# Optimization experiments

Hardware: AMD Instinct MI355X
Metric: run time of the kernel (lower is better)

## Reference

```python
import jax, jax.numpy as jnp
import numpy as np

B, L, D = 8, 4096, 256
G, K = 64, 8          # n_groups, group_size
N = G * K             # 512 slots
H = 8                 # attention heads
EPS = 1e-5

def _ln(x, g, b):
    m = jnp.mean(x, axis=-1, keepdims=True)
    v = jnp.var(x, axis=-1, keepdims=True)
    return (x - m) * jax.lax.rsqrt(v + EPS) * g + b

def _gelu(x):
    return jax.nn.gelu(x, approximate=False)  # torch nn.GELU default = exact erf

def setup_inputs() -> dict:
    key = jax.random.key(0)
    ks = jax.random.split(key, 24)
    s = 0.02
    d = {
        'X': jax.random.normal(ks[0], (B, L, D), jnp.float32),
        'S': jax.random.normal(ks[1], (B, N, D), jnp.float32),
        'Wg':  jax.random.normal(ks[2], (D, G)) * s,
        'Wk':  jax.random.normal(ks[3], (D, K)) * s,
        'Wm1': jax.random.normal(ks[4], (D, 2*D)) * s, 'bm1': jnp.zeros((2*D,)),
        'Wm2': jax.random.normal(ks[5], (2*D, D)) * s, 'bm2': jnp.zeros((D,)),
        'Wgt1': jax.random.normal(ks[6], (D, D)) * s, 'bgt1': jnp.zeros((D,)),
        'Wgt2': jax.random.normal(ks[7], (D, 1)) * s, 'bgt2': jnp.zeros((1,)),
        'Wqkv': jax.random.normal(ks[8], (D, 3*D)) * s, 'bqkv': jnp.zeros((3*D,)),
        'Wo':  jax.random.normal(ks[9], (D, D)) * s, 'bo': jnp.zeros((D,)),
        'aln_g': jnp.ones((D,)), 'aln_b': jnp.zeros((D,)),
        'Wu1': jax.random.normal(ks[10], (2*D, 2*D)) * s, 'bu1': jnp.zeros((2*D,)),
        'Wu2': jax.random.normal(ks[11], (2*D, D)) * s, 'bu2': jnp.zeros((D,)),
        'ln_g': jnp.ones((D,)), 'ln_b': jnp.zeros((D,)),
    }
    return d

def reference(X, S, Wg, Wk, Wm1, bm1, Wm2, bm2, Wgt1, bgt1, Wgt2, bgt2,
              Wqkv, bqkv, Wo, bo, aln_g, aln_b, Wu1, bu1, Wu2, bu2, ln_g, ln_b):
    # --- hierarchical routing (eval path: argmax one-hot) ---
    msg = _gelu(X @ Wm1 + bm1) @ Wm2 + bm2                 # (B,L,D)
    gate = jax.nn.sigmoid(_gelu(X @ Wgt1 + bgt1) @ Wgt2 + bgt2)  # (B,L,1)
    gm = msg * gate
    gidx = jnp.argmax(X @ Wg, axis=-1)                     # (B,L)
    kidx = jnp.argmax(X @ Wk, axis=-1)                     # (B,L)
    idx = gidx * K + kidx                                  # flat slot id in [0,N)
    full = jax.nn.one_hot(idx, N, dtype=X.dtype)           # (B,L,N)
    incoming = jnp.einsum('bln,bld->bnd', full, gm)        # (B,N,D)
    # --- slot self-attention ---
    qkv = S @ Wqkv + bqkv
    q, k, v = jnp.split(qkv, 3, axis=-1)
    dh = D // H
    q = q.reshape(B, N, H, dh); k = k.reshape(B, N, H, dh); v = v.reshape(B, N, H, dh)
    scores = jnp.einsum('bqhd,bkhd->bhqk', q, k) / jnp.sqrt(jnp.asarray(dh, X.dtype))
    attn = jax.nn.softmax(scores, axis=-1)
    o = jnp.einsum('bhqk,bkhd->bqhd', attn, v).reshape(B, N, D) @ Wo + bo
    S1 = _ln(S + o, aln_g, aln_b)
    # --- update ---
    cat = jnp.concatenate([S1, incoming], axis=-1)         # (B,N,2D)
    S2 = S1 + _gelu(cat @ Wu1 + bu1) @ Wu2 + bu2
    return _ln(S2, ln_g, ln_b)
```

## Files before the change

kernel.cpp:

```cpp
#include <hip/hip_runtime.h>

typedef __bf16 bf16_t;
typedef __bf16 bf16x8 __attribute__((ext_vector_type(8)));
typedef __bf16 bf16x4v __attribute__((ext_vector_type(4)));
typedef __bf16 bf16x2v __attribute__((ext_vector_type(2)));
typedef float f32x4 __attribute__((ext_vector_type(4)));
typedef unsigned long long u64;

#define LN_EPS 1e-5f

__device__ __forceinline__ float erf_fast(float a) {
  const float t = fabsf(a);
  const float s = a * a;
  float r;
  if (t > 0.921875f) {
    float u;
    r = fmaf(-1.72853470e-5f, t, 3.83197126e-4f);
    u = fmaf(-3.88396438e-3f, t, 2.42546219e-2f);
    r = fmaf(r, s, u);
    r = fmaf(r, t, 1.06777877e-1f);
    r = fmaf(r, t, -6.37245935e-1f);
    r = fmaf(r, t, -1.28717512e-1f);
    r = fmaf(r, t, t);
    r = 1.0f - __expf(-r);
    r = copysignf(r, a);
  } else {
    r = -5.96761703e-4f;
    r = fmaf(r, s, 4.99119423e-3f);
    r = fmaf(r, s, -2.67681349e-2f);
    r = fmaf(r, s, 1.12819925e-1f);
    r = fmaf(r, s, -3.76125336e-1f);
    r = fmaf(r, s, 1.28379166e-1f);
    r = fmaf(r, a, a);
  }
  return r;
}

__device__ __forceinline__ float gelu_f(float x) {
  const float h = 0.5f * x;
  return fmaf(h, erf_fast(x * 0.70710678118654752f), h);
}

__device__ __forceinline__ void async16(const bf16_t* g, bf16_t* l) {
  __builtin_amdgcn_global_load_lds(
      (const __attribute__((address_space(1))) void*)g,
      (__attribute__((address_space(3))) void*)l, 16, 0, 0);
}

__global__ __launch_bounds__(256)
void prep_kernel(const float* __restrict__ X, const float* __restrict__ S,
                 const float* __restrict__ Wg, const float* __restrict__ Wk,
                 const float* __restrict__ Wm1, const float* __restrict__ Wgt1,
                 const float* __restrict__ Wm2, const float* __restrict__ Wqkv,
                 const float* __restrict__ Wo, const float* __restrict__ Wu1,
                 const float* __restrict__ Wu2,
                 bf16_t* __restrict__ Xb, bf16_t* __restrict__ Sb,
                 bf16_t* __restrict__ W1t, bf16_t* __restrict__ W2t,
                 bf16_t* __restrict__ Wqkvt, bf16_t* __restrict__ Wot,
                 bf16_t* __restrict__ Wu1t, bf16_t* __restrict__ Wu2t,
                 float4* __restrict__ zbase)
{
  const int bid = blockIdx.x;
  const int t = threadIdx.x;
  if (bid < 2048) {
    const int base = bid * 1024 + t;
#pragma unroll
    for (int j = 0; j < 4; ++j) {
      const int i = base + j * 256;
      const float4 v = ((const float4*)X)[i];
      bf16x4v o; o[0]=(bf16_t)v.x; o[1]=(bf16_t)v.y; o[2]=(bf16_t)v.z; o[3]=(bf16_t)v.w;
      ((bf16x4v*)Xb)[i] = o;
    }
  } else if (bid < 2304) {
    const int base = (bid - 2048) * 1024 + t;
#pragma unroll
    for (int j = 0; j < 4; ++j) {
      const int i = base + j * 256;
      const float4 v = ((const float4*)S)[i];
      bf16x4v o; o[0]=(bf16_t)v.x; o[1]=(bf16_t)v.y; o[2]=(bf16_t)v.z; o[3]=(bf16_t)v.w;
      ((bf16x4v*)Sb)[i] = o;
    }
  } else if (bid < 3200) {
    const int n = bid - 2304;
    const int k = t;
    float v;
    if (n < 512)      v = Wm1[k * 512 + n];
    else if (n < 768) v = Wgt1[k * 256 + (n - 512)];
    else if (n < 832) v = Wg[k * 64 + (n - 768)];
    else if (n < 840) v = Wk[k * 8 + (n - 832)];
    else              v = 0.f;
    W1t[n * 256 + k] = (bf16_t)v;
  } else if (bid < 3456) {
    const int n = bid - 3200;
    for (int k = t; k < 512; k += 256) W2t[n * 512 + k] = (bf16_t)Wm2[k * 256 + n];
  } else if (bid < 4224) {
    const int n = bid - 3456;
    Wqkvt[n * 256 + t] = (bf16_t)Wqkv[t * 768 + n];
  } else if (bid < 4480) {
    const int n = bid - 4224;
    Wot[n * 256 + t] = (bf16_t)Wo[t * 256 + n];
  } else if (bid < 4992) {
    const int n = bid - 4480;
    for (int k = t; k < 512; k += 256) Wu1t[n * 512 + k] = (bf16_t)Wu1[k * 512 + n];
  } else if (bid < 5248) {
    const int n = bid - 4992;
    for (int k = t; k < 512; k += 256) Wu2t[n * 512 + k] = (bf16_t)Wu2[k * 256 + n];
  } else {
    const int base = (bid - 5248) * 1024 + t;
#pragma unroll
    for (int j = 0; j < 4; ++j)
      zbase[base + j * 256] = make_float4(0.f, 0.f, 0.f, 0.f);
  }
}

__global__ __launch_bounds__(256, 2)
void g1qkv_kernel(const bf16_t* __restrict__ A,
                  const bf16_t* __restrict__ Bt,
                  const float* __restrict__ bias, const float* __restrict__ bias2,
                  bf16_t* __restrict__ h1,
                  const float* __restrict__ wgt2, float* __restrict__ gatelin,
                  u64* __restrict__ bitmap,
                  const bf16_t* __restrict__ Sb, const bf16_t* __restrict__ Wqkvt,
                  const float* __restrict__ bqkv, bf16_t* __restrict__ qkvb,
                  bf16_t* __restrict__ Vt)
{
  const int bid = blockIdx.x;
  const int t = threadIdx.x;
  const int w = t >> 6;
  const int lane = t & 63;
  const int wr = w >> 1, wc = w & 1;
  const int quad = lane >> 4, l15 = lane & 15;

  __shared__ bf16_t lA[128 * 32];
  __shared__ bf16_t lB[128 * 32];
  __shared__ float sWg[256];
  __shared__ int sKi[128];

  if (bid >= 1792) {
    const int id = bid - 1792;
    const int m0 = (id & 63) * 64;
    const int n0 = (id >> 6) * 128;

    f32x4 acc[2][4];
#pragma unroll
    for (int mt = 0; mt < 2; ++mt)
#pragma unroll
      for (int nt = 0; nt < 4; ++nt)
        acc[mt][nt] = (f32x4){0.f, 0.f, 0.f, 0.f};

    for (int k0 = 0; k0 < 256; k0 += 32) {
      async16(Sb + (size_t)(m0 + (t >> 2)) * 256 + k0 + (t & 3) * 8,
              lA + (size_t)(t & 192) * 8);
#pragma unroll
      for (int i = 0; i < 2; ++i) {
        const int c = i * 256 + t;
        async16(Wqkvt + (size_t)(n0 + (c >> 2)) * 256 + k0 + (c & 3) * 8,
                lB + (size_t)(i * 256 + (t & 192)) * 8);
      }
      __syncthreads();
      bf16x8 af[2], bfr[4];
      const int ko = quad * 8;
#pragma unroll
      for (int mt = 0; mt < 2; ++mt)
        af[mt] = *(const bf16x8*)&lA[(wr * 32 + mt * 16 + l15) * 32 + ko];
#pragma unroll
      for (int nt = 0; nt < 4; ++nt)
        bfr[nt] = *(const bf16x8*)&lB[(wc * 64 + nt * 16 + l15) * 32 + ko];
#pragma unroll
      for (int mt = 0; mt < 2; ++mt)
#pragma unroll
        for (int nt = 0; nt < 4; ++nt)
          acc[mt][nt] = __builtin_amdgcn_mfma_f32_16x16x32_bf16(bfr[nt], af[mt], acc[mt][nt], 0, 0, 0);
      __syncthreads();
    }

    if (n0 < 512) {
#pragma unroll
      for (int mt = 0; mt < 2; ++mt) {
        const int row = m0 + wr * 32 + mt * 16 + l15;
#pragma unroll
        for (int nt = 0; nt < 4; ++nt) {
          const int colb = n0 + wc * 64 + nt * 16 + quad * 4;
          const float4 bb = *(const float4*)&bqkv[colb];
          bf16x4v o; o[0]=(bf16_t)(acc[mt][nt][0]+bb.x); o[1]=(bf16_t)(acc[mt][nt][1]+bb.y);
          o[2]=(bf16_t)(acc[mt][nt][2]+bb.z); o[3]=(bf16_t)(acc[mt][nt][3]+bb.w);
          *(bf16x4v*)&qkvb[(size_t)row * 768 + colb] = o;
        }
      }
    } else {
#pragma unroll
      for (int mt = 0; mt < 2; ++mt) {
        const int row = m0 + wr * 32 + mt * 16 + l15;
        const int b = row >> 9, key = row & 511;
#pragma unroll
        for (int nt = 0; nt < 4; ++nt) {
          const int colb = n0 + wc * 64 + nt * 16 + quad * 4;
          const int c = colb - 512;
          const int h2 = c >> 5, dh = c & 31;
          const float4 bb = *(const float4*)&bqkv[colb];
          bf16_t* vb = Vt + ((size_t)(b * 8 + h2) * 32 + dh) * 512 + key;
          vb[0]   = (bf16_t)(acc[mt][nt][0] + bb.x);
          vb[512] = (bf16_t)(acc[mt][nt][1] + bb.y);
          vb[1024]= (bf16_t)(acc[mt][nt][2] + bb.z);
          vb[1536]= (bf16_t)(acc[mt][nt][3] + bb.w);
        }
      }
    }
    return;
  }

  const int m0 = (bid & 255) * 128;
  const int by = bid >> 8;
  const int n0 = by * 128;

  if (by >= 4 && by < 6) sWg[t] = wgt2[t];

  f32x4 acc[4][4];
#pragma unroll
  for (int mt = 0; mt < 4; ++mt)
#pragma unroll
    for (int nt = 0; nt < 4; ++nt)
      acc[mt][nt] = (f32x4){0.f, 0.f, 0.f, 0.f};

  const int srow = t >> 2;
  const int schunk = ((t & 3) ^ (srow & 3)) * 8;
  const int ko = ((quad ^ (l15 & 3)) << 3);

  for (int k0 = 0; k0 < 256; k0 += 32) {
#pragma unroll
    for (int i = 0; i < 2; ++i) {
      const int row = i * 64 + srow;
      async16(A + (size_t)(m0 + row) * 256 + k0 + schunk,
              lA + (size_t)(i * 256 + (t & 192)) * 8);
      async16(Bt + (size_t)(n0 + row) * 256 + k0 + schunk,
              lB + (size_t)(i * 256 + (t & 192)) * 8);
    }
    __syncthreads();
    bf16x8 af[4], bfr[4];
#pragma unroll
    for (int mt = 0; mt < 4; ++mt)
      af[mt] = *(const bf16x8*)&lA[(wr * 64 + mt * 16 + l15) * 32 + ko];
#pragma unroll
    for (int nt = 0; nt < 4; ++nt)
      bfr[nt] = *(const bf16x8*)&lB[(wc * 64 + nt * 16 + l15) * 32 + ko];
#pragma unroll
    for (int mt = 0; mt < 4; ++mt)
#pragma unroll
      for (int nt = 0; nt < 4; ++nt)
        acc[mt][nt] = __builtin_amdgcn_mfma_f32_16x16x32_bf16(bfr[nt], af[mt], acc[mt][nt], 0, 0, 0);
    __syncthreads();
  }

  if (by < 4) {
#pragma unroll
    for (int mt = 0; mt < 4; ++mt) {
      const int row = m0 + wr * 64 + mt * 16 + l15;
#pragma unroll
      for (int nt = 0; nt < 4; ++nt) {
        const int colb = n0 + wc * 64 + nt * 16 + quad * 4;
        const float4 bb = *(const float4*)&bias[colb];
        bf16x4v o;
        o[0] = (bf16_t)gelu_f(acc[mt][nt][0] + bb.x);
        o[1] = (bf16_t)gelu_f(acc[mt][nt][1] + bb.y);
        o[2] = (bf16_t)gelu_f(acc[mt][nt][2] + bb.z);
        o[3] = (bf16_t)gelu_f(acc[mt][nt][3] + bb.w);
        *(bf16x4v*)&h1[(size_t)row * 512 + colb] = o;
      }
    }
  } else if (by < 6) {
#pragma unroll
    for (int mt = 0; mt < 4; ++mt) {
      const int row = m0 + wr * 64 + mt * 16 + l15;
      float part = 0.f;
#pragma unroll
      for (int nt = 0; nt < 4; ++nt) {
        const int colb = n0 + wc * 64 + nt * 16 + quad * 4;
        const int c = colb - 512;
        const float4 bb = *(const float4*)&bias2[c];
        part = fmaf(gelu_f(acc[mt][nt][0] + bb.x), sWg[c + 0], part);
        part = fmaf(gelu_f(acc[mt][nt][1] + bb.y), sWg[c + 1], part);
        part = fmaf(gelu_f(acc[mt][nt][2] + bb.z), sWg[c + 2], part);
        part = fmaf(gelu_f(acc[mt][nt][3] + bb.w), sWg[c + 3], part);
      }
      part += __shfl_xor(part, 16, 64);
      part += __shfl_xor(part, 32, 64);
      if (lane < 16) atomicAdd(&gatelin[row], part);
    }
  } else {
    int bi[4];
#pragma unroll
    for (int mt = 0; mt < 4; ++mt) {
      if (wc == 0) {
        float mv = -1e30f; int mi = 0;
#pragma unroll
        for (int nt = 0; nt < 4; ++nt)
#pragma unroll
          for (int j = 0; j < 4; ++j) {
            const int gc = nt * 16 + quad * 4 + j;
            const float v = acc[mt][nt][j];
            if (v > mv || (v == mv && gc < mi)) { mv = v; mi = gc; }
          }
#pragma unroll
        for (int off = 16; off <= 32; off <<= 1) {
          const float ov = __shfl_xor(mv, off, 64);
          const int oi = __shfl_xor(mi, off, 64);
          if (ov > mv || (ov == mv && oi < mi)) { mv = ov; mi = oi; }
        }
        bi[mt] = mi;
      } else {
        float mv = -1e30f; int mi = 0;
        if (quad < 2) {
#pragma unroll
          for (int j = 0; j < 4; ++j) {
            const int kc = quad * 4 + j;
            const float v = acc[mt][0][j];
            if (v > mv || (v == mv && kc < mi)) { mv = v; mi = kc; }
          }
        }
#pragma unroll
        for (int off = 16; off <= 32; off <<= 1) {
          const float ov = __shfl_xor(mv, off, 64);
          const int oi = __shfl_xor(mi, off, 64);
          if (ov > mv || (ov == mv && oi < mi)) { mv = ov; mi = oi; }
        }
        if (lane < 16) sKi[wr * 64 + mt * 16 + l15] = mi;
      }
    }
    __syncthreads();
    if (wc == 0 && lane < 16) {
#pragma unroll
      for (int mt = 0; mt < 4; ++mt) {
        const int rl = wr * 64 + mt * 16 + l15;
        const int row = m0 + rl;
        const int idx = bi[mt] * 8 + sKi[rl];
        const int b = row >> 12, tok = row & 4095;
        atomicOr(&bitmap[(size_t)(b * 512 + idx) * 64 + (tok >> 6)],
                 1ull << (tok & 63));
      }
    }
  }
}

__global__ __launch_bounds__(256)
void gather_kernel(const bf16_t* __restrict__ h1, const float* __restrict__ gatelin,
                   const float* __restrict__ bgt2, const u64* __restrict__ bitmap,
                   bf16_t* __restrict__ H, float* __restrict__ sumg)
{
  const int bs = blockIdx.x;
  const int b = bs >> 9;
  const int t = threadIdx.x;
  const int w = t >> 6, lane = t & 63;
  __shared__ u64 sw[64];
  __shared__ float pa[4][512];
  __shared__ float psg[4];
  if (t < 64) sw[t] = bitmap[(size_t)bs * 64 + t];
  __syncthreads();
  const float bg = bgt2[0];

  float a[8];
#pragma unroll
  for (int j = 0; j < 8; ++j) a[j] = 0.f;
  float sg = 0.f;

  int wd = w * 16;
  const int wend = wd + 16;
  u64 word = sw[wd];
  auto pop = [&]() -> int {
    while (word == 0) {
      if (++wd >= wend) return -1;
      word = sw[wd];
    }
    const int bit = __builtin_ctzll(word);
    word &= word - 1;
    return (b << 12) + (wd << 6) + bit;
  };

  int l0 = pop();
  float gl0 = 0.f;
  bf16x8 hv0 = {};
  if (l0 >= 0) {
    gl0 = gatelin[l0];
    hv0 = *(const bf16x8*)&h1[(size_t)l0 * 512 + lane * 8];
  }
  while (l0 >= 0) {
    const int l1 = pop();
    float gl1 = 0.f;
    bf16x8 hv1 = {};
    if (l1 >= 0) {
      gl1 = gatelin[l1];
      hv1 = *(const bf16x8*)&h1[(size_t)l1 * 512 + lane * 8];
    }
    const float g = 1.0f / (1.0f + __expf(-(gl0 + bg)));
#pragma unroll
    for (int j = 0; j < 8; ++j) a[j] = fmaf(g, (float)hv0[j], a[j]);
    sg += g;
    l0 = l1; gl0 = gl1; hv0 = hv1;
  }

#pragma unroll
  for (int j = 0; j < 8; ++j) pa[w][lane * 8 + j] = a[j];
  if (lane == 0) psg[w] = sg;
  __syncthreads();

  const int c = t * 2;
  const float r0 = pa[0][c] + pa[1][c] + pa[2][c] + pa[3][c];
  const float r1 = pa[0][c + 1] + pa[1][c + 1] + pa[2][c + 1] + pa[3][c + 1];
  bf16x2v o; o[0] = (bf16_t)r0; o[1] = (bf16_t)r1;
  *(bf16x2v*)&H[(size_t)bs * 512 + c] = o;
  if (t == 0) sumg[bs] = psg[0] + psg[1] + psg[2] + psg[3];
}

__global__ __launch_bounds__(256)
void g2attn_kernel(const bf16_t* __restrict__ qkv, const bf16_t* __restrict__ Vt,
                   bf16_t* __restrict__ obuf,
                   const bf16_t* __restrict__ H, const bf16_t* __restrict__ W2t,
                   const float* __restrict__ bm2, const float* __restrict__ sumg,
                   float* __restrict__ incom)
{
  const int bid = blockIdx.x;
  const int t = threadIdx.x;
  const int w = t >> 6, lane = t & 63;
  const int quad = lane >> 4, l15 = lane & 15;

  __shared__ bf16_t sP[32 * 520];
  __shared__ float sL[32];

  if (bid < 128) {
    const int wr = w >> 1, wc = w & 1;
    const int m0 = (bid & 63) * 64;
    const int n0 = (bid >> 6) * 128;
    bf16_t* lA = sP;
    bf16_t* lB = sP + 64 * 32;

    f32x4 acc[2][4];
#pragma unroll
    for (int mt = 0; mt < 2; ++mt)
#pragma unroll
      for (int nt = 0; nt < 4; ++nt)
        acc[mt][nt] = (f32x4){0.f, 0.f, 0.f, 0.f};

    for (int k0 = 0; k0 < 512; k0 += 32) {
      async16(H + (size_t)(m0 + (t >> 2)) * 512 + k0 + (t & 3) * 8,
              lA + (size_t)(t & 192) * 8);
#pragma unroll
      for (int i = 0; i < 2; ++i) {
        const int c = i * 256 + t;
        async16(W2t + (size_t)(n0 + (c >> 2)) * 512 + k0 + (c & 3) * 8,
                lB + (size_t)(i * 256 + (t & 192)) * 8);
      }
      __syncthreads();
      bf16x8 af[2], bfr[4];
      const int ko = quad * 8;
#pragma unroll
      for (int mt = 0; mt < 2; ++mt)
        af[mt] = *(const bf16x8*)&lA[(wr * 32 + mt * 16 + l15) * 32 + ko];
#pragma unroll
      for (int nt = 0; nt < 4; ++nt)
        bfr[nt] = *(const bf16x8*)&lB[(wc * 64 + nt * 16 + l15) * 32 + ko];
#pragma unroll
      for (int mt = 0; mt < 2; ++mt)
#pragma unroll
        for (int nt = 0; nt < 4; ++nt)
          acc[mt][nt] = __builtin_amdgcn_mfma_f32_16x16x32_bf16(bfr[nt], af[mt], acc[mt][nt], 0, 0, 0);
      __syncthreads();
    }

#pragma unroll
    for (int mt = 0; mt < 2; ++mt) {
      const int row = m0 + wr * 32 + mt * 16 + l15;
      const float gt = sumg[row];
#pragma unroll
      for (int nt = 0; nt < 4; ++nt) {
        const int colb = n0 + wc * 64 + nt * 16 + quad * 4;
        const float4 bb = *(const float4*)&bm2[colb];
        *(float4*)&incom[(size_t)row * 256 + colb] =
            make_float4(fmaf(gt, bb.x, acc[mt][nt][0]), fmaf(gt, bb.y, acc[mt][nt][1]),
                        fmaf(gt, bb.z, acc[mt][nt][2]), fmaf(gt, bb.w, acc[mt][nt][3]));
      }
    }
    return;
  }

  const int abid = bid - 128;
  const int qc = abid & 15;
  const int h = (abid >> 4) & 7;
  const int b = abid >> 7;

  bf16x8 qf[2];
#pragma unroll
  for (int mt = 0; mt < 2; ++mt) {
    const int row = b * 512 + qc * 32 + mt * 16 + l15;
    qf[mt] = *(const bf16x8*)&qkv[(size_t)row * 768 + h * 32 + quad * 8];
  }
  const float scale = 0.17677669529663687f;
  for (int kt = w; kt < 32; kt += 4) {
    const int key = b * 512 + kt * 16 + l15;
    const bf16x8 kf = *(const bf16x8*)&qkv[(size_t)key * 768 + 256 + h * 32 + quad * 8];
#pragma unroll
    for (int mt = 0; mt < 2; ++mt) {
      f32x4 c = (f32x4){0.f, 0.f, 0.f, 0.f};
      c = __builtin_amdgcn_mfma_f32_16x16x32_bf16(qf[mt], kf, c, 0, 0, 0);
#pragma unroll
      for (int r = 0; r < 4; ++r)
        sP[(mt * 16 + quad * 4 + r) * 520 + kt * 16 + l15] = (bf16_t)(c[r] * scale);
    }
  }
  __syncthreads();

#pragma unroll
  for (int ri = 0; ri < 8; ++ri) {
    const int row = w * 8 + ri;
    const bf16x8 sv = *(const bf16x8*)&sP[row * 520 + lane * 8];
    float sval[8];
    float mx = -1e30f;
#pragma unroll
    for (int j = 0; j < 8; ++j) { sval[j] = (float)sv[j]; mx = fmaxf(mx, sval[j]); }
#pragma unroll
    for (int off = 32; off; off >>= 1) mx = fmaxf(mx, __shfl_xor(mx, off, 64));
    float sum = 0.f;
    bf16x8 pv;
#pragma unroll
    for (int j = 0; j < 8; ++j) { const float e = __expf(sval[j] - mx); sum += e; pv[j] = (bf16_t)e; }
#pragma unroll
    for (int off = 32; off; off >>= 1) sum += __shfl_xor(sum, off, 64);
    *(bf16x8*)&sP[row * 520 + lane * 8] = pv;
    if (lane == 0) sL[row] = sum;
  }
  __syncthreads();

  const int wq = w >> 1, wd = w & 1;
  const bf16_t* vbase = Vt + ((size_t)(b * 8 + h) * 32 + wd * 16 + l15) * 512;
  const bf16_t* pbase = &sP[(wq * 16 + l15) * 520];
  f32x4 oacc = (f32x4){0.f, 0.f, 0.f, 0.f};
#pragma unroll
  for (int kt = 0; kt < 16; ++kt) {
    const bf16x8 af = *(const bf16x8*)&pbase[kt * 32 + quad * 8];
    const bf16x8 vf = *(const bf16x8*)&vbase[kt * 32 + quad * 8];
    oacc = __builtin_amdgcn_mfma_f32_16x16x32_bf16(vf, af, oacc, 0, 0, 0);
  }
  const int rowq = wq * 16 + l15;
  const float inv = 1.0f / sL[rowq];
  bf16x4v o;
#pragma unroll
  for (int r = 0; r < 4; ++r) o[r] = (bf16_t)(oacc[r] * inv);
  *(bf16x4v*)&obuf[(size_t)(b * 512 + qc * 32 + rowq) * 256 + h * 32 + wd * 16 + quad * 4] = o;
}

__global__ __launch_bounds__(256)
void tail_kernel(const bf16_t* __restrict__ obuf, const bf16_t* __restrict__ Wot,
                 const float* __restrict__ bo, const float* __restrict__ S,
                 const float* __restrict__ incom,
                 const float* __restrict__ g1n, const float* __restrict__ b1n,
                 const bf16_t* __restrict__ Wu1t, const float* __restrict__ bu1,
                 const bf16_t* __restrict__ Wu2t, const float* __restrict__ bu2,
                 const float* __restrict__ g2n, const float* __restrict__ b2n,
                 float* __restrict__ out)
{
  const int m0 = blockIdx.x * 16;
  const int t = threadIdx.x;
  const int w = t >> 6, lane = t & 63;
  const int quad = lane >> 4, l15 = lane & 15;

  __shared__ bf16_t lB[512 * 32];
  __shared__ bf16_t lA[16 * 32];
  __shared__ bf16_t A4s[16 * 520];
  __shared__ bf16_t Us[16 * 520];
  __shared__ float sSum[4][16];
  __shared__ float sSq[4][16];

  const int schunk = ((t & 3) ^ ((t >> 2) & 3)) * 8;
  const int ko_b = ((quad ^ (l15 & 3)) << 3);
  const int ko_a = quad * 8;
  const int row = m0 + l15;

  {
    f32x4 acc[4];
#pragma unroll
    for (int nt = 0; nt < 4; ++nt) acc[nt] = (f32x4){0.f, 0.f, 0.f, 0.f};

    for (int k0 = 0; k0 < 256; k0 += 32) {
      if (t < 64)
        async16(obuf + (size_t)(m0 + (t >> 2)) * 256 + k0 + (t & 3) * 8, lA);
#pragma unroll
      for (int i = 0; i < 4; ++i) {
        const int c = i * 256 + t;
        async16(Wot + (size_t)(c >> 2) * 256 + k0 + schunk,
                lB + (size_t)(i * 256 + (t & 192)) * 8);
      }
      __syncthreads();
      const bf16x8 af = *(const bf16x8*)&lA[l15 * 32 + ko_a];
#pragma unroll
      for (int nt = 0; nt < 4; ++nt) {
        const bf16x8 bfr = *(const bf16x8*)&lB[(w * 64 + nt * 16 + l15) * 32 + ko_b];
        acc[nt] = __builtin_amdgcn_mfma_f32_16x16x32_bf16(bfr, af, acc[nt], 0, 0, 0);
      }
      __syncthreads();
    }

    float sum = 0.f, sq = 0.f;
#pragma unroll
    for (int nt = 0; nt < 4; ++nt) {
      const int colb = w * 64 + nt * 16 + quad * 4;
      const float4 bv = *(const float4*)&bo[colb];
      const float4 sv = *(const float4*)&S[(size_t)row * 256 + colb];
      float x0 = acc[nt][0] + bv.x + sv.x, x1 = acc[nt][1] + bv.y + sv.y;
      float x2 = acc[nt][2] + bv.z + sv.z, x3 = acc[nt][3] + bv.w + sv.w;
      acc[nt][0] = x0; acc[nt][1] = x1; acc[nt][2] = x2; acc[nt][3] = x3;
      sum += x0 + x1 + x2 + x3;
      sq += x0*x0 + x1*x1 + x2*x2 + x3*x3;
    }
    sum += __shfl_xor(sum, 16, 64); sum += __shfl_xor(sum, 32, 64);
    sq  += __shfl_xor(sq, 16, 64);  sq  += __shfl_xor(sq, 32, 64);
    if (lane < 16) { sSum[w][l15] = sum; sSq[w][l15] = sq; }
    __syncthreads();
    const float tot = sSum[0][l15] + sSum[1][l15] + sSum[2][l15] + sSum[3][l15];
    const float tq  = sSq[0][l15] + sSq[1][l15] + sSq[2][l15] + sSq[3][l15];
    const float mean = tot * 0.00390625f;
    const float var = tq * 0.00390625f - mean * mean;
    const float rstd = rsqrtf(var + LN_EPS);
#pragma unroll
    for (int nt = 0; nt < 4; ++nt) {
      const int colb = w * 64 + nt * 16 + quad * 4;
      const float4 gg = *(const float4*)&g1n[colb];
      const float4 bv = *(const float4*)&b1n[colb];
      bf16x4v yb;
      yb[0] = (bf16_t)((acc[nt][0]-mean)*rstd*gg.x + bv.x);
      yb[1] = (bf16_t)((acc[nt][1]-mean)*rstd*gg.y + bv.y);
      yb[2] = (bf16_t)((acc[nt][2]-mean)*rstd*gg.z + bv.z);
      yb[3] = (bf16_t)((acc[nt][3]-mean)*rstd*gg.w + bv.w);
      *(bf16x4v*)&A4s[l15 * 520 + colb] = yb;
      const float4 ic = *(const float4*)&incom[(size_t)row * 256 + colb];
      bf16x4v ib; ib[0]=(bf16_t)ic.x; ib[1]=(bf16_t)ic.y; ib[2]=(bf16_t)ic.z; ib[3]=(bf16_t)ic.w;
      *(bf16x4v*)&A4s[l15 * 520 + 256 + colb] = ib;
    }
  }
  __syncthreads();

  {
    f32x4 acc2[8];
#pragma unroll
    for (int nt = 0; nt < 8; ++nt) acc2[nt] = (f32x4){0.f, 0.f, 0.f, 0.f};

    for (int k0 = 0; k0 < 512; k0 += 32) {
#pragma unroll
      for (int i = 0; i < 8; ++i) {
        const int c = i * 256 + t;
        async16(Wu1t + (size_t)(c >> 2) * 512 + k0 + schunk,
                lB + (size_t)(i * 256 + (t & 192)) * 8);
      }
      __syncthreads();
      const bf16x8 af = *(const bf16x8*)&A4s[l15 * 520 + k0 + ko_a];
#pragma unroll
      for (int nt = 0; nt < 8; ++nt) {
        const bf16x8 bfr = *(const bf16x8*)&lB[(w * 128 + nt * 16 + l15) * 32 + ko_b];
        acc2[nt] = __builtin_amdgcn_mfma_f32_16x16x32_bf16(bfr, af, acc2[nt], 0, 0, 0);
      }
      __syncthreads();
    }
#pragma unroll
    for (int nt = 0; nt < 8; ++nt) {
      const int colb = w * 128 + nt * 16 + quad * 4;
      const float4 bb = *(const float4*)&bu1[colb];
      bf16x4v o;
      o[0] = (bf16_t)gelu_f(acc2[nt][0] + bb.x);
      o[1] = (bf16_t)gelu_f(acc2[nt][1] + bb.y);
      o[2] = (bf16_t)gelu_f(acc2[nt][2] + bb.z);
      o[3] = (bf16_t)gelu_f(acc2[nt][3] + bb.w);
      *(bf16x4v*)&Us[l15 * 520 + colb] = o;
    }
  }
  __syncthreads();

  {
    f32x4 acc3[4];
#pragma unroll
    for (int nt = 0; nt < 4; ++nt) acc3[nt] = (f32x4){0.f, 0.f, 0.f, 0.f};

    for (int k0 = 0; k0 < 512; k0 += 32) {
#pragma unroll
      for (int i = 0; i < 4; ++i) {
        const int c = i * 256 + t;
        async16(Wu2t + (size_t)(c >> 2) * 512 + k0 + schunk,
                lB + (size_t)(i * 256 + (t & 192)) * 8);
      }
      __syncthreads();
      const bf16x8 af = *(const bf16x8*)&Us[l15 * 520 + k0 + ko_a];
#pragma unroll
      for (int nt = 0; nt < 4; ++nt) {
        const bf16x8 bfr = *(const bf16x8*)&lB[(w * 64 + nt * 16 + l15) * 32 + ko_b];
        acc3[nt] = __builtin_amdgcn_mfma_f32_16x16x32_bf16(bfr, af, acc3[nt], 0, 0, 0);
      }
      __syncthreads();
    }

    float sum = 0.f, sq = 0.f;
#pragma unroll
    for (int nt = 0; nt < 4; ++nt) {
      const int colb = w * 64 + nt * 16 + quad * 4;
      const float4 bv = *(const float4*)&bu2[colb];
      const bf16x4v s1v = *(const bf16x4v*)&A4s[l15 * 520 + colb];
      float x0 = acc3[nt][0] + bv.x + (float)s1v[0];
      float x1 = acc3[nt][1] + bv.y + (float)s1v[1];
      float x2 = acc3[nt][2] + bv.z + (float)s1v[2];
      float x3 = acc3[nt][3] + bv.w + (float)s1v[3];
      acc3[nt][0] = x0; acc3[nt][1] = x1; acc3[nt][2] = x2; acc3[nt][3] = x3;
      sum += x0 + x1 + x2 + x3;
      sq += x0*x0 + x1*x1 + x2*x2 + x3*x3;
    }
    sum += __shfl_xor(sum, 16, 64); sum += __shfl_xor(sum, 32, 64);
    sq  += __shfl_xor(sq, 16, 64);  sq  += __shfl_xor(sq, 32, 64);
    __syncthreads();
    if (lane < 16) { sSum[w][l15] = sum; sSq[w][l15] = sq; }
    __syncthreads();
    const float tot = sSum[0][l15] + sSum[1][l15] + sSum[2][l15] + sSum[3][l15];
    const float tq  = sSq[0][l15] + sSq[1][l15] + sSq[2][l15] + sSq[3][l15];
    const float mean = tot * 0.00390625f;
    const float var = tq * 0.00390625f - mean * mean;
    const float rstd = rsqrtf(var + LN_EPS);
#pragma unroll
    for (int nt = 0; nt < 4; ++nt) {
      const int colb = w * 64 + nt * 16 + quad * 4;
      const float4 gg = *(const float4*)&g2n[colb];
      const float4 bv = *(const float4*)&b2n[colb];
      *(float4*)&out[(size_t)row * 256 + colb] = make_float4(
          (acc3[nt][0]-mean)*rstd*gg.x + bv.x, (acc3[nt][1]-mean)*rstd*gg.y + bv.y,
          (acc3[nt][2]-mean)*rstd*gg.z + bv.z, (acc3[nt][3]-mean)*rstd*gg.w + bv.w);
    }
  }
}

extern "C" void kernel_launch(void* const* d_in, const int* in_sizes, int n_in,
                              void* d_out, int out_size, void* d_ws, size_t ws_size,
                              hipStream_t stream)
{
  (void)in_sizes; (void)n_in; (void)out_size; (void)ws_size;
  const float* X    = (const float*)d_in[0];
  const float* S    = (const float*)d_in[1];
  const float* Wg   = (const float*)d_in[2];
  const float* Wk   = (const float*)d_in[3];
  const float* Wm1  = (const float*)d_in[4];
  const float* bm1  = (const float*)d_in[5];
  const float* Wm2  = (const float*)d_in[6];
  const float* bm2  = (const float*)d_in[7];
  const float* Wgt1 = (const float*)d_in[8];
  const float* bgt1 = (const float*)d_in[9];
  const float* Wgt2 = (const float*)d_in[10];
  const float* bgt2 = (const float*)d_in[11];
  const float* Wqkv = (const float*)d_in[12];
  const float* bqkv = (const float*)d_in[13];
  const float* Wo   = (const float*)d_in[14];
  const float* bo   = (const float*)d_in[15];
  const float* alng = (const float*)d_in[16];
  const float* alnb = (const float*)d_in[17];
  const float* Wu1  = (const float*)d_in[18];
  const float* bu1  = (const float*)d_in[19];
  const float* Wu2  = (const float*)d_in[20];
  const float* bu2  = (const float*)d_in[21];
  const float* lng  = (const float*)d_in[22];
  const float* lnb  = (const float*)d_in[23];

  char* p = (char*)d_ws;
  auto carve = [&](size_t bytes) { char* r = p; p += bytes; return r; };
  bf16_t* Xb    = (bf16_t*)carve(16777216);
  bf16_t* Sb    = (bf16_t*)carve(2097152);
  bf16_t* W1t   = (bf16_t*)carve(458752);
  bf16_t* W2t   = (bf16_t*)carve(262144);
  bf16_t* Wqkvt = (bf16_t*)carve(393216);
  bf16_t* Wot   = (bf16_t*)carve(131072);
  bf16_t* Wu1t  = (bf16_t*)carve(524288);
  bf16_t* Wu2t  = (bf16_t*)carve(262144);
  bf16_t* h1    = (bf16_t*)carve(33554432);
  u64*    bitmap  = (u64*)carve(2097152);
  float*  gatelin = (float*)carve(131072);
  float*  incom = (float*)carve(4194304);
  bf16_t* qkvb  = (bf16_t*)carve(6291456);
  bf16_t* Vt    = (bf16_t*)carve(2097152);
  bf16_t* obuf  = (bf16_t*)carve(2097152);
  bf16_t* H     = (bf16_t*)carve(4194304);
  float*  sumg  = (float*)carve(16384);

  prep_kernel<<<5384, 256, 0, stream>>>(X, S, Wg, Wk, Wm1, Wgt1, Wm2, Wqkv, Wo, Wu1, Wu2,
                                        Xb, Sb, W1t, W2t, Wqkvt, Wot, Wu1t, Wu2t,
                                        (float4*)bitmap);
  g1qkv_kernel<<<2176, 256, 0, stream>>>(Xb, W1t, bm1, bgt1, h1,
                                         Wgt2, gatelin, bitmap,
                                         Sb, Wqkvt, bqkv, qkvb, Vt);
  gather_kernel<<<4096, 256, 0, stream>>>(h1, gatelin, bgt2, bitmap, H, sumg);
  g2attn_kernel<<<1152, 256, 0, stream>>>(qkvb, Vt, obuf,
                                          H, W2t, bm2, sumg, incom);
  tail_kernel<<<256, 256, 0, stream>>>(obuf, Wot, bo, S, incom, alng, alnb,
                                       Wu1t, bu1, Wu2t, bu2, lng, lnb,
                                       (float*)d_out);
}
```

Baseline: 258.3 us.

## Fuse gather with attention and move message GEMM into tail kernel

Merges the gather kernel and the attention half of g2attn into one launch. Blocks 0-4095 do the gated gather and the rest do slot attention. The H·W2 message projection moves into tail_kernel, which computes the incoming rows directly into shared memory. This removes a kernel launch and the fp32 incom round-trip through global memory. In exchange, the tail kernel's 256 blocks each redo a 16-row by 256-column GEMM with K=512, which lengthens that low-occupancy critical stage.

```diff
diff --git a/kernel.cpp b/kernel.cpp
--- a/kernel.cpp
+++ b/kernel.cpp
@@ -342,146 +342,85 @@
 }
 
 __global__ __launch_bounds__(256)
-void gather_kernel(const bf16_t* __restrict__ h1, const float* __restrict__ gatelin,
-                   const float* __restrict__ bgt2, const u64* __restrict__ bitmap,
-                   bf16_t* __restrict__ H, float* __restrict__ sumg)
+void gatherattn_kernel(const bf16_t* __restrict__ h1, const float* __restrict__ gatelin,
+                       const float* __restrict__ bgt2, const u64* __restrict__ bitmap,
+                       bf16_t* __restrict__ Hout, float* __restrict__ sumg,
+                       const bf16_t* __restrict__ qkv, const bf16_t* __restrict__ Vt,
+                       bf16_t* __restrict__ obuf)
 {
-  const int bs = blockIdx.x;
-  const int b = bs >> 9;
-  const int t = threadIdx.x;
-  const int w = t >> 6, lane = t & 63;
-  __shared__ u64 sw[64];
-  __shared__ float pa[4][512];
-  __shared__ float psg[4];
-  if (t < 64) sw[t] = bitmap[(size_t)bs * 64 + t];
-  __syncthreads();
-  const float bg = bgt2[0];
-
-  float a[8];
-#pragma unroll
-  for (int j = 0; j < 8; ++j) a[j] = 0.f;
-  float sg = 0.f;
-
-  int wd = w * 16;
-  const int wend = wd + 16;
-  u64 word = sw[wd];
-  auto pop = [&]() -> int {
-    while (word == 0) {
-      if (++wd >= wend) return -1;
-      word = sw[wd];
-    }
-    const int bit = __builtin_ctzll(word);
-    word &= word - 1;
-    return (b << 12) + (wd << 6) + bit;
-  };
-
-  int l0 = pop();
-  float gl0 = 0.f;
-  bf16x8 hv0 = {};
-  if (l0 >= 0) {
-    gl0 = gatelin[l0];
-    hv0 = *(const bf16x8*)&h1[(size_t)l0 * 512 + lane * 8];
-  }
-  while (l0 >= 0) {
-    const int l1 = pop();
-    float gl1 = 0.f;
-    bf16x8 hv1 = {};
-    if (l1 >= 0) {
-      gl1 = gatelin[l1];
-      hv1 = *(const bf16x8*)&h1[(size_t)l1 * 512 + lane * 8];
-    }
-    const float g = 1.0f / (1.0f + __expf(-(gl0 + bg)));
-#pragma unroll
-    for (int j = 0; j < 8; ++j) a[j] = fmaf(g, (float)hv0[j], a[j]);
-    sg += g;
-    l0 = l1; gl0 = gl1; hv0 = hv1;
-  }
-
-#pragma unroll
-  for (int j = 0; j < 8; ++j) pa[w][lane * 8 + j] = a[j];
-  if (lane == 0) psg[w] = sg;
-  __syncthreads();
-
-  const int c = t * 2;
-  const float r0 = pa[0][c] + pa[1][c] + pa[2][c] + pa[3][c];
-  const float r1 = pa[0][c + 1] + pa[1][c + 1] + pa[2][c + 1] + pa[3][c + 1];
-  bf16x2v o; o[0] = (bf16_t)r0; o[1] = (bf16_t)r1;
-  *(bf16x2v*)&H[(size_t)bs * 512 + c] = o;
-  if (t == 0) sumg[bs] = psg[0] + psg[1] + psg[2] + psg[3];
-}
-
-__global__ __launch_bounds__(256)
-void g2attn_kernel(const bf16_t* __restrict__ qkv, const bf16_t* __restrict__ Vt,
-                   bf16_t* __restrict__ obuf,
-                   const bf16_t* __restrict__ H, const bf16_t* __restrict__ W2t,
-                   const float* __restrict__ bm2, const float* __restrict__ sumg,
-                   float* __restrict__ incom)
-{
+  __shared__ __align__(16) char smem[33536];
   const int bid = blockIdx.x;
   const int t = threadIdx.x;
   const int w = t >> 6, lane = t & 63;
   const int quad = lane >> 4, l15 = lane & 15;
 
-  __shared__ bf16_t sP[32 * 520];
-  __shared__ float sL[32];
-
-  if (bid < 128) {
-    const int wr = w >> 1, wc = w & 1;
-    const int m0 = (bid & 63) * 64;
-    const int n0 = (bid >> 6) * 128;
-    bf16_t* lA = sP;
-    bf16_t* lB = sP + 64 * 32;
-
-    f32x4 acc[2][4];
-#pragma unroll
-    for (int mt = 0; mt < 2; ++mt)
-#pragma unroll
-      for (int nt = 0; nt < 4; ++nt)
-        acc[mt][nt] = (f32x4){0.f, 0.f, 0.f, 0.f};
-
-    for (int k0 = 0; k0 < 512; k0 += 32) {
-      async16(H + (size_t)(m0 + (t >> 2)) * 512 + k0 + (t & 3) * 8,
-              lA + (size_t)(t & 192) * 8);
-#pragma unroll
-      for (int i = 0; i < 2; ++i) {
-        const int c = i * 256 + t;
-        async16(W2t + (size_t)(n0 + (c >> 2)) * 512 + k0 + (c & 3) * 8,
-                lB + (size_t)(i * 256 + (t & 192)) * 8);
-      }
-      __syncthreads();
-      bf16x8 af[2], bfr[4];
-      const int ko = quad * 8;
-#pragma unroll
-      for (int mt = 0; mt < 2; ++mt)
-        af[mt] = *(const bf16x8*)&lA[(wr * 32 + mt * 16 + l15) * 32 + ko];
-#pragma unroll
-      for (int nt = 0; nt < 4; ++nt)
-        bfr[nt] = *(const bf16x8*)&lB[(wc * 64 + nt * 16 + l15) * 32 + ko];
-#pragma unroll
-      for (int mt = 0; mt < 2; ++mt)
-#pragma unroll
-        for (int nt = 0; nt < 4; ++nt)
-          acc[mt][nt] = __builtin_amdgcn_mfma_f32_16x16x32_bf16(bfr[nt], af[mt], acc[mt][nt], 0, 0, 0);
-      __syncthreads();
-    }
-
-#pragma unroll
-    for (int mt = 0; mt < 2; ++mt) {
-      const int row = m0 + wr * 32 + mt * 16 + l15;
-      const float gt = sumg[row];
-#pragma unroll
-      for (int nt = 0; nt < 4; ++nt) {
-        const int colb = n0 + wc * 64 + nt * 16 + quad * 4;
-        const float4 bb = *(const float4*)&bm2[colb];
-        *(float4*)&incom[(size_t)row * 256 + colb] =
-            make_float4(fmaf(gt, bb.x, acc[mt][nt][0]), fmaf(gt, bb.y, acc[mt][nt][1]),
-                        fmaf(gt, bb.z, acc[mt][nt][2]), fmaf(gt, bb.w, acc[mt][nt][3]));
-      }
-    }
+  if (bid < 4096) {
+    u64* sw = (u64*)smem;
+    float* pa = (float*)(smem + 512);
+    float* psg = (float*)(smem + 512 + 8192);
+    const int bs = bid;
+    const int b = bs >> 9;
+    if (t < 64) sw[t] = bitmap[(size_t)bs * 64 + t];
+    __syncthreads();
+    const float bg = bgt2[0];
+
+    float a[8];
+#pragma unroll
+    for (int j = 0; j < 8; ++j) a[j] = 0.f;
+    float sg = 0.f;
+
+    int wd = w * 16;
+    const int wend = wd + 16;
+    u64 word = sw[wd];
+    auto pop = [&]() -> int {
+      while (word == 0) {
+        if (++wd >= wend) return -1;
+        word = sw[wd];
+      }
+      const int bit = __builtin_ctzll(word);
+      word &= word - 1;
+      return (b << 12) + (wd << 6) + bit;
+    };
+
+    int l0 = pop();
+    float gl0 = 0.f;
+    bf16x8 hv0 = {};
+    if (l0 >= 0) {
+      gl0 = gatelin[l0];
+      hv0 = *(const bf16x8*)&h1[(size_t)l0 * 512 + lane * 8];
+    }
+    while (l0 >= 0) {
+      const int l1 = pop();
+      float gl1 = 0.f;
+      bf16x8 hv1 = {};
+      if (l1 >= 0) {
+        gl1 = gatelin[l1];
+        hv1 = *(const bf16x8*)&h1[(size_t)l1 * 512 + lane * 8];
+      }
+      const float g = 1.0f / (1.0f + __expf(-(gl0 + bg)));
+#pragma unroll
+      for (int j = 0; j < 8; ++j) a[j] = fmaf(g, (float)hv0[j], a[j]);
+      sg += g;
+      l0 = l1; gl0 = gl1; hv0 = hv1;
+    }
+
+#pragma unroll
+    for (int j = 0; j < 8; ++j) pa[w * 512 + lane * 8 + j] = a[j];
+    if (lane == 0) psg[w] = sg;
+    __syncthreads();
+
+    const int c = t * 2;
+    const float r0 = pa[c] + pa[512 + c] + pa[1024 + c] + pa[1536 + c];
+    const float r1 = pa[c + 1] + pa[512 + c + 1] + pa[1024 + c + 1] + pa[1536 + c + 1];
+    bf16x2v o; o[0] = (bf16_t)r0; o[1] = (bf16_t)r1;
+    *(bf16x2v*)&Hout[(size_t)bs * 512 + c] = o;
+    if (t == 0) sumg[bs] = psg[0] + psg[1] + psg[2] + psg[3];
     return;
   }
 
-  const int abid = bid - 128;
+  bf16_t* sP = (bf16_t*)smem;
+  float* sL = (float*)(smem + 33280);
+  const int abid = bid - 4096;
   const int qc = abid & 15;
   const int h = (abid >> 4) & 7;
   const int b = abid >> 7;
@@ -549,11 +488,12 @@
 __global__ __launch_bounds__(256)
 void tail_kernel(const bf16_t* __restrict__ obuf, const bf16_t* __restrict__ Wot,
                  const float* __restrict__ bo, const float* __restrict__ S,
-                 const float* __restrict__ incom,
                  const float* __restrict__ g1n, const float* __restrict__ b1n,
                  const bf16_t* __restrict__ Wu1t, const float* __restrict__ bu1,
                  const bf16_t* __restrict__ Wu2t, const float* __restrict__ bu2,
                  const float* __restrict__ g2n, const float* __restrict__ b2n,
+                 const bf16_t* __restrict__ H, const bf16_t* __restrict__ W2t,
+                 const float* __restrict__ bm2, const float* __restrict__ sumg,
                  float* __restrict__ out)
 {
   const int m0 = blockIdx.x * 16;
@@ -572,6 +512,44 @@
   const int ko_b = ((quad ^ (l15 & 3)) << 3);
   const int ko_a = quad * 8;
   const int row = m0 + l15;
+
+  {
+    f32x4 acc0[4];
+#pragma unroll
+    for (int nt = 0; nt < 4; ++nt) acc0[nt] = (f32x4){0.f, 0.f, 0.f, 0.f};
+
+    for (int k0 = 0; k0 < 512; k0 += 32) {
+      if (t < 64)
+        async16(H + (size_t)(m0 + (t >> 2)) * 512 + k0 + (t & 3) * 8, lA);
+#pragma unroll
+      for (int i = 0; i < 4; ++i) {
+        const int c = i * 256 + t;
+        async16(W2t + (size_t)(c >> 2) * 512 + k0 + schunk,
+                lB + (size_t)(i * 256 + (t & 192)) * 8);
+      }
+      __syncthreads();
+      const bf16x8 af = *(const bf16x8*)&lA[l15 * 32 + ko_a];
+#pragma unroll
+      for (int nt = 0; nt < 4; ++nt) {
+        const bf16x8 bfr = *(const bf16x8*)&lB[(w * 64 + nt * 16 + l15) * 32 + ko_b];
+        acc0[nt] = __builtin_amdgcn_mfma_f32_16x16x32_bf16(bfr, af, acc0[nt], 0, 0, 0);
+      }
+      __syncthreads();
+    }
+    const float gt = sumg[row];
+#pragma unroll
+    for (int nt = 0; nt < 4; ++nt) {
+      const int colb = w * 64 + nt * 16 + quad * 4;
+      const float4 bb = *(const float4*)&bm2[colb];
+      bf16x4v ib;
+      ib[0] = (bf16_t)fmaf(gt, bb.x, acc0[nt][0]);
+      ib[1] = (bf16_t)fmaf(gt, bb.y, acc0[nt][1]);
+      ib[2] = (bf16_t)fmaf(gt, bb.z, acc0[nt][2]);
+      ib[3] = (bf16_t)fmaf(gt, bb.w, acc0[nt][3]);
+      *(bf16x4v*)&A4s[l15 * 520 + 256 + colb] = ib;
+    }
+  }
+  __syncthreads();
 
   {
     f32x4 acc[4];
@@ -629,9 +607,6 @@
       yb[2] = (bf16_t)((acc[nt][2]-mean)*rstd*gg.z + bv.z);
       yb[3] = (bf16_t)((acc[nt][3]-mean)*rstd*gg.w + bv.w);
       *(bf16x4v*)&A4s[l15 * 520 + colb] = yb;
-      const float4 ic = *(const float4*)&incom[(size_t)row * 256 + colb];
-      bf16x4v ib; ib[0]=(bf16_t)ic.x; ib[1]=(bf16_t)ic.y; ib[2]=(bf16_t)ic.z; ib[3]=(bf16_t)ic.w;
-      *(bf16x4v*)&A4s[l15 * 520 + 256 + colb] = ib;
     }
   }
   __syncthreads();
@@ -772,7 +747,6 @@
   bf16_t* h1    = (bf16_t*)carve(33554432);
   u64*    bitmap  = (u64*)carve(2097152);
   float*  gatelin = (float*)carve(131072);
-  float*  incom = (float*)carve(4194304);
   bf16_t* qkvb  = (bf16_t*)carve(6291456);
   bf16_t* Vt    = (bf16_t*)carve(2097152);
   bf16_t* obuf  = (bf16_t*)carve(2097152);
@@ -785,10 +759,10 @@
   g1qkv_kernel<<<2176, 256, 0, stream>>>(Xb, W1t, bm1, bgt1, h1,
                                          Wgt2, gatelin, bitmap,
                                          Sb, Wqkvt, bqkv, qkvb, Vt);
-  gather_kernel<<<4096, 256, 0, stream>>>(h1, gatelin, bgt2, bitmap, H, sumg);
-  g2attn_kernel<<<1152, 256, 0, stream>>>(qkvb, Vt, obuf,
-                                          H, W2t, bm2, sumg, incom);
-  tail_kernel<<<256, 256, 0, stream>>>(obuf, Wot, bo, S, incom, alng, alnb,
+  gatherattn_kernel<<<5120, 256, 0, stream>>>(h1, gatelin, bgt2, bitmap, H, sumg,
+                                              qkvb, Vt, obuf);
+  tail_kernel<<<256, 256, 0, stream>>>(obuf, Wot, bo, S, alng, alnb,
                                        Wu1t, bu1, Wu2t, bu2, lng, lnb,
+                                       H, W2t, bm2, sumg,
                                        (float*)d_out);
 }
```

Result: faster. 244.8 us (-5.2%).
